# Kernel optimization log

Measured on AMD Instinct MI355X. Metric: run time of the kernel, lower is better.

Reference implementation:

```python
import jax, jax.numpy as jnp
import numpy as np

DIM = 128
HEADS = 4
GN_GROUPS = 4
EPS = 1e-5


def setup_inputs() -> dict:
    key = jax.random.key(0)
    ks = jax.random.split(key, 6)
    B, C, H, W = 4, DIM, 64, 64
    x = jax.random.normal(ks[0], (B, C, H, W), dtype=jnp.float32)
    # 1x1 convs are channel matmuls: store as [out_ch, in_ch]
    w_qkv = jax.random.normal(ks[1], (3 * C, C), dtype=jnp.float32) * (C ** -0.5)
    w_out = jax.random.normal(ks[2], (C, C), dtype=jnp.float32) * (C ** -0.5)
    b_out = jax.random.normal(ks[3], (C,), dtype=jnp.float32) * 0.01
    gn_gamma = jnp.ones((C,), dtype=jnp.float32)
    gn_beta = jnp.zeros((C,), dtype=jnp.float32)
    return {"x": x, "w_qkv": w_qkv, "w_out": w_out, "b_out": b_out,
            "gn_gamma": gn_gamma, "gn_beta": gn_beta}


def _attention_block(x, w_qkv, w_out, b_out, gn_gamma, gn_beta):
    b, c, h, w = x.shape
    d = c // HEADS
    scale = d ** -0.5
    # 1x1 conv == per-pixel matmul over channels
    qkv = jnp.einsum('bchw,oc->bohw', x, w_qkv)  # [b, 3c, h, w]
    q, k, v = jnp.split(qkv, 3, axis=1)
    # 'b (h d) x y -> b h (x y) d'
    def to_heads(t):
        return t.reshape(b, HEADS, d, h * w).transpose(0, 1, 3, 2)  # [b, H, N, d]
    q, k, v = to_heads(q), to_heads(k), to_heads(v)
    dots = jnp.einsum('bhnd,bhmd->bhnm', q, k) * scale  # [b, H, N, N]
    attn = jax.nn.softmax(dots, axis=-1)
    out = jnp.einsum('bhnm,bhmd->bhnd', attn, v)  # [b, H, N, d]
    # 'b h (x y) d -> b (h d) x y'
    out = out.transpose(0, 1, 3, 2).reshape(b, c, h, w)
    # output 1x1 conv + bias
    out = jnp.einsum('bchw,oc->bohw', out, w_out) + b_out[None, :, None, None]
    # GroupNorm(4, c)
    g = out.reshape(b, GN_GROUPS, c // GN_GROUPS, h, w)
    mean = g.mean(axis=(2, 3, 4), keepdims=True)
    var = g.var(axis=(2, 3, 4), keepdims=True)
    g = (g - mean) * jax.lax.rsqrt(var + EPS)
    out = g.reshape(b, c, h, w) * gn_gamma[None, :, None, None] + gn_beta[None, :, None, None]
    return out + x


def reference(x, w_qkv, w_out, b_out, gn_gamma, gn_beta):
    return _attention_block(x, w_qkv, w_out, b_out, gn_gamma, gn_beta)
```

## Files before the change

kernel.cpp:

```cpp
#include <hip/hip_runtime.h>

#define DIM   128
#define NPIX  4096
#define DHEAD 32

using u16 = unsigned short;
typedef __attribute__((ext_vector_type(8))) short   short8;
typedef __attribute__((ext_vector_type(8))) u16     ushort8;
typedef __attribute__((ext_vector_type(4))) float   floatx4;
typedef __attribute__((ext_vector_type(2))) unsigned int uint2v;

#define SCL 0.25513899f

__device__ __forceinline__ float bf2f(u16 u) {
  union { unsigned int i; float f; } v; v.i = ((unsigned int)u) << 16; return v.f;
}
__device__ __forceinline__ u16 f2bf(float f) {
  union { unsigned int i; float f; } v; v.f = f;
  unsigned int i = v.i;
  return (u16)((i + 0x7FFFu + ((i >> 16) & 1u)) >> 16);
}
__device__ __forceinline__ unsigned int pk2bf(float a, float b) {
  union { float f; unsigned int u; } ua, ub; ua.f = a; ub.f = b;
  return __builtin_amdgcn_perm(ub.u, ua.u, 0x07060302u);
}

template<bool F32> __device__ __forceinline__ float ld1(const void* p, size_t i) {
  if constexpr (F32) return ((const float*)p)[i];
  else               return bf2f(((const u16*)p)[i]);
}
template<bool F32> __device__ __forceinline__ float4 ld4(const void* p, size_t i) {
  if constexpr (F32) {
    return *(const float4*)((const float*)p + i);
  } else {
    const ushort4 u = *(const ushort4*)((const u16*)p + i);
    return make_float4(bf2f(u.x), bf2f(u.y), bf2f(u.z), bf2f(u.w));
  }
}
template<bool F32> __device__ __forceinline__ void st4(void* p, size_t i, float4 v) {
  if constexpr (F32) {
    *(float4*)((float*)p + i) = v;
  } else {
    ushort4 u; u.x = f2bf(v.x); u.y = f2bf(v.y); u.z = f2bf(v.z); u.w = f2bf(v.w);
    *(ushort4*)((u16*)p + i) = u;
  }
}

__global__ void k_detect(const u16* __restrict__ x, int* __restrict__ flag,
                         float* __restrict__ S) {
  if (threadIdx.x < 40) S[threadIdx.x] = 0.f;
  if (threadIdx.x == 0 && blockIdx.x == 0) {
    int big = 0;
    for (int i = 0; i < 128; ++i) {
      const float v = bf2f(x[i]);
      if (!(fabsf(v) < 1e4f)) big = 1;
    }
    *flag = big;
  }
}

template<bool F32>
__global__ __launch_bounds__(256) void k_qkv(const void* __restrict__ x,
                                             const void* __restrict__ wqkv,
                                             u16* __restrict__ Q,
                                             u16* __restrict__ K,
                                             u16* __restrict__ V,
                                             const int* __restrict__ flag) {
  if (*flag != (F32 ? 1 : 0)) return;
  const int b = blockIdx.z, y = blockIdx.y, pt = blockIdx.x;
  const int tl = threadIdx.x;
  __shared__ float Ws[32 * 129];
  if (y < 8) {
    const int m = y >> 2, h = y & 3;
    const int ddq = tl & 3, pw = tl >> 2;
    const int rb = m * DIM + h * 32;
    for (int i = tl; i < 32 * DIM; i += 256)
      Ws[(i >> 7) * 129 + (i & 127)] =
          ld1<F32>(wqkv, (size_t)(rb + (i >> 7)) * DIM + (i & 127));
    __syncthreads();
    const int p0 = pt * 256 + pw * 4;
    float acc[8][4];
#pragma unroll
    for (int j = 0; j < 8; ++j) { acc[j][0] = acc[j][1] = acc[j][2] = acc[j][3] = 0.f; }
    const size_t xb = (size_t)b * DIM * NPIX + p0;
    for (int c = 0; c < DIM; ++c) {
      const float4 xv = ld4<F32>(x, xb + (size_t)c * NPIX);
#pragma unroll
      for (int j = 0; j < 8; ++j) {
        const float wv = Ws[(ddq * 8 + j) * 129 + c];
        acc[j][0] += wv * xv.x; acc[j][1] += wv * xv.y;
        acc[j][2] += wv * xv.z; acc[j][3] += wv * xv.w;
      }
    }
    u16* dst = (m == 0) ? Q : K;
    const float scl = (m == 0) ? 1.f : SCL;
    const int bh = b * 4 + h;
#pragma unroll
    for (int t = 0; t < 4; ++t) {
      ushort8 w8;
#pragma unroll
      for (int j = 0; j < 8; ++j) w8[j] = f2bf(acc[j][t] * scl);
      *(ushort8*)(dst + ((size_t)bh * NPIX + p0 + t) * DHEAD + ddq * 8) = w8;
    }
  } else {
    const int og = (y - 8) * 4 + (pt >> 2);
    const int ptv = pt & 3;
    for (int i = tl; i < 8 * DIM; i += 256)
      Ws[(i >> 7) * 129 + (i & 127)] =
          ld1<F32>(wqkv, (size_t)(2 * DIM + og * 8 + (i >> 7)) * DIM + (i & 127));
    __syncthreads();
    const int p0 = ptv * 1024 + tl * 4;
    float acc[8][4];
#pragma unroll
    for (int j = 0; j < 8; ++j) { acc[j][0] = acc[j][1] = acc[j][2] = acc[j][3] = 0.f; }
    const size_t xb = (size_t)b * DIM * NPIX + p0;
    for (int c = 0; c < DIM; ++c) {
      const float4 xv = ld4<F32>(x, xb + (size_t)c * NPIX);
#pragma unroll
      for (int j = 0; j < 8; ++j) {
        const float wv = Ws[j * 129 + c];
        acc[j][0] += wv * xv.x; acc[j][1] += wv * xv.y;
        acc[j][2] += wv * xv.z; acc[j][3] += wv * xv.w;
      }
    }
#pragma unroll
    for (int j = 0; j < 8; ++j) {
      const int c = og * 8 + j;
      ushort4 w4;
      w4.x = f2bf(acc[j][0]); w4.y = f2bf(acc[j][1]);
      w4.z = f2bf(acc[j][2]); w4.w = f2bf(acc[j][3]);
      *(ushort4*)(V + ((size_t)b * DIM + c) * NPIX + p0) = w4;
    }
  }
}

__device__ __forceinline__ short8 xform_p(unsigned c0, unsigned c1,
                                          unsigned c2, unsigned c3) {
  uint2v sw = __builtin_amdgcn_permlane32_swap(c0, c2, false, false);
  uint2v sx = __builtin_amdgcn_permlane16_swap(sw[0], sw[1], false, false);
  uint2v sy = __builtin_amdgcn_permlane32_swap(c1, c3, false, false);
  uint2v sz = __builtin_amdgcn_permlane16_swap(sy[0], sy[1], false, false);
  union { unsigned u[4]; short8 s; } r;
  r.u[0] = sx[0]; r.u[1] = sz[0]; r.u[2] = sx[1]; r.u[3] = sz[1];
  return r.s;
}

__global__ __launch_bounds__(512) void k_attn(const u16* __restrict__ Q,
                                              const u16* __restrict__ K,
                                              const u16* __restrict__ V,
                                              u16* __restrict__ O) {
  const int id = blockIdx.y * 32 + blockIdx.x;
  const int nid = (id & 7) * 64 + (id >> 3);
  const int bh = nid >> 5, qb = nid & 31;
  const int tid = threadIdx.x;
  const int wv = tid >> 6, lane = tid & 63;
  const int quad = lane >> 4, l15 = lane & 15;
  const int b = bh >> 2, h = bh & 3;

  __shared__ __align__(16) u16 Klds[2][128 * 40];
  __shared__ __align__(16) u16 Vlds[2][32 * 136];
  __shared__ __align__(16) u16 Olds[32 * 136];

  const int qtok0 = qb * 128 + wv * 16 + l15;
  const short8 qf = *(const short8*)(Q + ((size_t)bh * NPIX + qtok0) * DHEAD + quad * 8);

  floatx4 o00 = {0.f, 0.f, 0.f, 0.f}, o01 = {0.f, 0.f, 0.f, 0.f};
  floatx4 ol  = {0.f, 0.f, 0.f, 0.f};
  const short8 onesf = {(short)0x3F80, (short)0x3F80, (short)0x3F80, (short)0x3F80,
                        (short)0x3F80, (short)0x3F80, (short)0x3F80, (short)0x3F80};

  const int st = tid & 255;
  const bool isK = tid < 256;
  const int skey = st >> 2, sqt = st & 3;
  const int sdd = st >> 3, soc = st & 7;
  const u16* Gg = isK ? (K + ((size_t)bh * NPIX + skey) * DHEAD + sqt * 8)
                      : (V + ((size_t)(b * DIM + h * DHEAD + sdd)) * NPIX + soc * 8);
  u16* Ld0 = isK ? (Klds[0] + skey * 40 + sqt * 8) : (Vlds[0] + sdd * 136 + soc * 8);
  u16* Ld1 = isK ? (Klds[1] + skey * 40 + sqt * 8) : (Vlds[1] + sdd * 136 + soc * 8);
  const size_t gstep = isK ? (size_t)(128 * DHEAD) : (size_t)128;
  const size_t goff2 = isK ? (size_t)(64 * DHEAD)  : (size_t)64;
  const int    loff2 = isK ? (64 * 40) : 64;

  *(ushort8*)Ld0           = *(const ushort8*)Gg;
  *(ushort8*)(Ld0 + loff2) = *(const ushort8*)(Gg + goff2);

  for (int ch = 0; ch < 32; ++ch) {
    const int cur = ch & 1;
    __syncthreads();
    ushort8 pre0, pre1;
    if (ch + 1 < 32) {
      const u16* gb = Gg + (size_t)(ch + 1) * gstep;
      pre0 = *(const ushort8*)gb;
      pre1 = *(const ushort8*)(gb + goff2);
    }
#pragma unroll
    for (int kc = 0; kc < 4; ++kc) {
      unsigned ca[4];
#pragma unroll
      for (int s = 0; s < 2; ++s) {
        const int sub = kc * 2 + s;
        const short8 af = *(const short8*)(Klds[cur] + (sub * 16 + l15) * 40 + quad * 8);
        const floatx4 s0 = __builtin_amdgcn_mfma_f32_16x16x32_bf16(
            af, qf, (floatx4){0.f, 0.f, 0.f, 0.f}, 0, 0, 0);
        const float a0 = __builtin_amdgcn_exp2f(s0[0]);
        const float a1 = __builtin_amdgcn_exp2f(s0[1]);
        const float a2 = __builtin_amdgcn_exp2f(s0[2]);
        const float a3 = __builtin_amdgcn_exp2f(s0[3]);
        ca[s * 2 + 0] = pk2bf(a0, a1); ca[s * 2 + 1] = pk2bf(a2, a3);
      }
      const short8 pa = xform_p(ca[0], ca[1], ca[2], ca[3]);
      const short8 vb0 = *(const short8*)(Vlds[cur] + l15 * 136 + kc * 32 + quad * 8);
      const short8 vb1 = *(const short8*)(Vlds[cur] + (16 + l15) * 136 + kc * 32 + quad * 8);
      __builtin_amdgcn_s_setprio(1);
      o00 = __builtin_amdgcn_mfma_f32_16x16x32_bf16(pa, vb0, o00, 0, 0, 0);
      o01 = __builtin_amdgcn_mfma_f32_16x16x32_bf16(pa, vb1, o01, 0, 0, 0);
      ol  = __builtin_amdgcn_mfma_f32_16x16x32_bf16(pa, onesf, ol, 0, 0, 0);
      __builtin_amdgcn_s_setprio(0);
    }
    if (ch + 1 < 32) {
      u16* dst = cur ? Ld0 : Ld1;
      *(ushort8*)dst           = pre0;
      *(ushort8*)(dst + loff2) = pre1;
    }
  }
  float li[4];
#pragma unroll
  for (int r = 0; r < 4; ++r) li[r] = 1.f / ol[r];
  uint2v w00, w01;
  w00[0] = (unsigned)f2bf(o00[0] * li[0]) | ((unsigned)f2bf(o00[1] * li[1]) << 16);
  w00[1] = (unsigned)f2bf(o00[2] * li[2]) | ((unsigned)f2bf(o00[3] * li[3]) << 16);
  w01[0] = (unsigned)f2bf(o01[0] * li[0]) | ((unsigned)f2bf(o01[1] * li[1]) << 16);
  w01[1] = (unsigned)f2bf(o01[2] * li[2]) | ((unsigned)f2bf(o01[3] * li[3]) << 16);
  __syncthreads();
  *(uint2v*)(Olds + l15 * 136 + wv * 16 + quad * 4) = w00;
  *(uint2v*)(Olds + (16 + l15) * 136 + wv * 16 + quad * 4) = w01;
  __syncthreads();
  const int d = tid >> 4, oc = tid & 15;
  u16* og = O + ((size_t)(b * DIM + h * DHEAD + d)) * NPIX + qb * 128;
  *(ushort8*)(og + oc * 8) = *(const ushort8*)(Olds + d * 136 + oc * 8);
}

template<bool F32>
__global__ __launch_bounds__(256) void k_proj(const u16* __restrict__ O,
                                              const void* __restrict__ wout,
                                              const void* __restrict__ bout,
                                              float* __restrict__ Y,
                                              float* __restrict__ Sred,
                                              const int* __restrict__ flag) {
  if (*flag != (F32 ? 1 : 0)) return;
  const int b = blockIdx.z, og = blockIdx.y, pt = blockIdx.x;
  const int tl = threadIdx.x;
  __shared__ float Ws[8][DIM];
  for (int i = tl; i < 8 * DIM; i += 256)
    Ws[i >> 7][i & 127] = ld1<F32>(wout, (size_t)(og * 8 + (i >> 7)) * DIM + (i & 127));
  __syncthreads();
  const int p0 = pt * 512 + tl * 2;
  float acc[8][2];
#pragma unroll
  for (int j = 0; j < 8; ++j) { acc[j][0] = acc[j][1] = 0.f; }
  const u16* Ob = O + (size_t)b * DIM * NPIX + p0;
  for (int c = 0; c < DIM; ++c) {
    const ushort2 xv2 = *(const ushort2*)(Ob + (size_t)c * NPIX);
    const float x0 = bf2f(xv2.x), x1 = bf2f(xv2.y);
#pragma unroll
    for (int j = 0; j < 8; ++j) {
      const float wv = Ws[j][c];
      acc[j][0] += wv * x0; acc[j][1] += wv * x1;
    }
  }
  float s1 = 0.f, s2 = 0.f;
#pragma unroll
  for (int j = 0; j < 8; ++j) {
    const int o = og * 8 + j;
    const float bo = ld1<F32>(bout, o);
    float2 y2;
    y2.x = acc[j][0] + bo; y2.y = acc[j][1] + bo;
    *(float2*)(Y + ((size_t)b * DIM + o) * NPIX + p0) = y2;
    s1 += y2.x + y2.y;
    s2 += y2.x * y2.x + y2.y * y2.y;
  }
  __shared__ float red[2][256];
  red[0][tl] = s1; red[1][tl] = s2;
  __syncthreads();
  for (int off = 128; off >= 1; off >>= 1) {
    if (tl < off) { red[0][tl] += red[0][tl + off]; red[1][tl] += red[1][tl + off]; }
    __syncthreads();
  }
  if (tl == 0) {
    const int g = og >> 2;
    atomicAdd(&Sred[(b * 4 + g) * 2 + 0], red[0][0]);
    atomicAdd(&Sred[(b * 4 + g) * 2 + 1], red[1][0]);
  }
}

template<bool F32>
__global__ __launch_bounds__(256) void k_gn(const float* __restrict__ Y,
                                            const float* __restrict__ Sred,
                                            const void* __restrict__ x,
                                            const void* __restrict__ gamma,
                                            const void* __restrict__ beta,
                                            void* __restrict__ out,
                                            const int* __restrict__ flag) {
  if (*flag != (F32 ? 1 : 0)) return;
  const int idx = (blockIdx.x * 256 + threadIdx.x) * 4;
  const int b = idx >> 19;
  const int c = (idx >> 12) & 127;
  const int g = c >> 5;
  const float inv_n = 1.f / (32.f * 4096.f);
  const float s1 = Sred[(b * 4 + g) * 2 + 0];
  const float s2 = Sred[(b * 4 + g) * 2 + 1];
  const float mean = s1 * inv_n;
  const float var = s2 * inv_n - mean * mean;
  const float rs = rsqrtf(var + 1e-5f);
  const float ga = ld1<F32>(gamma, c) * rs;
  const float be = ld1<F32>(beta, c) - mean * ga;
  const float4 y4 = *(const float4*)(Y + idx);
  const float4 xv = ld4<F32>(x, idx);
  float4 r;
  r.x = y4.x * ga + be + xv.x;
  r.y = y4.y * ga + be + xv.y;
  r.z = y4.z * ga + be + xv.z;
  r.w = y4.w * ga + be + xv.w;
  st4<F32>(out, idx, r);
}

extern "C" void kernel_launch(void* const* d_in, const int* in_sizes, int n_in,
                              void* d_out, int out_size, void* d_ws, size_t ws_size,
                              hipStream_t stream) {
  const void* x     = d_in[0];
  const void* wqkv  = d_in[1];
  const void* wout  = d_in[2];
  const void* bout  = d_in[3];
  const void* gamma = d_in[4];
  const void* beta  = d_in[5];
  char* ws = (char*)d_ws;
  u16*   Q = (u16*)(ws + ((size_t)0  << 20));
  u16*   K = (u16*)(ws + ((size_t)8  << 20));
  u16*   V = (u16*)(ws + ((size_t)16 << 20));
  u16*   O = (u16*)(ws + ((size_t)24 << 20));
  float* Y = (float*)(ws + ((size_t)32 << 20));
  float* S = (float*)(ws + ((size_t)40 << 20));
  int*   F = (int*)(ws + ((size_t)40 << 20) + 128);

  k_detect<<<1, 64, 0, stream>>>((const u16*)x, F, S);

  k_qkv<false><<<dim3(16, 12, 4), 256, 0, stream>>>(x, wqkv, Q, K, V, F);
  k_qkv<true> <<<dim3(16, 12, 4), 256, 0, stream>>>(x, wqkv, Q, K, V, F);
  k_attn<<<dim3(32, 16), 512, 0, stream>>>(Q, K, V, O);
  k_proj<false><<<dim3(8, 16, 4), 256, 0, stream>>>(O, wout, bout, Y, S, F);
  k_proj<true> <<<dim3(8, 16, 4), 256, 0, stream>>>(O, wout, bout, Y, S, F);
  k_gn<false><<<2048, 256, 0, stream>>>(Y, S, x, gamma, beta, d_out, F);
  k_gn<true> <<<2048, 256, 0, stream>>>(Y, S, x, gamma, beta, d_out, F);
}
```

Measured before the change: 180.4 us.

## Fuse GroupNorm and residual into projection kernel with grid-wide atomic barrier

Drops the separate GroupNorm kernel and the fp32 intermediate Y buffer. The projection kernel keeps its outputs in registers and publishes group sums by atomics. Each block then spins on a global counter until all 512 blocks have contributed, and applies normalization, gamma/beta and the residual before writing the output directly. This removes a full round trip of the projection output through global memory plus one launch. In exchange it relies on all 512 blocks being co-resident to avoid deadlock, and adds spin-wait latency.

Result: slower. 210.7 us (+16.8%).

```diff
diff --git a/kernel.cpp b/kernel.cpp
--- a/kernel.cpp
+++ b/kernel.cpp
@@ -37,12 +37,20 @@
     return make_float4(bf2f(u.x), bf2f(u.y), bf2f(u.z), bf2f(u.w));
   }
 }
-template<bool F32> __device__ __forceinline__ void st4(void* p, size_t i, float4 v) {
+template<bool F32> __device__ __forceinline__ float2 ld2(const void* p, size_t i) {
   if constexpr (F32) {
-    *(float4*)((float*)p + i) = v;
+    return *(const float2*)((const float*)p + i);
   } else {
-    ushort4 u; u.x = f2bf(v.x); u.y = f2bf(v.y); u.z = f2bf(v.z); u.w = f2bf(v.w);
-    *(ushort4*)((u16*)p + i) = u;
+    const ushort2 u = *(const ushort2*)((const u16*)p + i);
+    return make_float2(bf2f(u.x), bf2f(u.y));
+  }
+}
+template<bool F32> __device__ __forceinline__ void st2(void* p, size_t i, float2 v) {
+  if constexpr (F32) {
+    *(float2*)((float*)p + i) = v;
+  } else {
+    ushort2 u; u.x = f2bf(v.x); u.y = f2bf(v.y);
+    *(ushort2*)((u16*)p + i) = u;
   }
 }
 
@@ -244,8 +252,12 @@
 __global__ __launch_bounds__(256) void k_proj(const u16* __restrict__ O,
                                               const void* __restrict__ wout,
                                               const void* __restrict__ bout,
-                                              float* __restrict__ Y,
+                                              const void* __restrict__ x,
+                                              const void* __restrict__ gamma,
+                                              const void* __restrict__ beta,
+                                              void* __restrict__ out,
                                               float* __restrict__ Sred,
+                                              int* __restrict__ Ctr,
                                               const int* __restrict__ flag) {
   if (*flag != (F32 ? 1 : 0)) return;
   const int b = blockIdx.z, og = blockIdx.y, pt = blockIdx.x;
@@ -271,13 +283,10 @@
   float s1 = 0.f, s2 = 0.f;
 #pragma unroll
   for (int j = 0; j < 8; ++j) {
-    const int o = og * 8 + j;
-    const float bo = ld1<F32>(bout, o);
-    float2 y2;
-    y2.x = acc[j][0] + bo; y2.y = acc[j][1] + bo;
-    *(float2*)(Y + ((size_t)b * DIM + o) * NPIX + p0) = y2;
-    s1 += y2.x + y2.y;
-    s2 += y2.x * y2.x + y2.y * y2.y;
+    const float bo = ld1<F32>(bout, og * 8 + j);
+    acc[j][0] += bo; acc[j][1] += bo;
+    s1 += acc[j][0] + acc[j][1];
+    s2 += acc[j][0] * acc[j][0] + acc[j][1] * acc[j][1];
   }
   __shared__ float red[2][256];
   red[0][tl] = s1; red[1][tl] = s2;
@@ -286,42 +295,35 @@
     if (tl < off) { red[0][tl] += red[0][tl + off]; red[1][tl] += red[1][tl + off]; }
     __syncthreads();
   }
+  const int g = og >> 2;
   if (tl == 0) {
-    const int g = og >> 2;
     atomicAdd(&Sred[(b * 4 + g) * 2 + 0], red[0][0]);
     atomicAdd(&Sred[(b * 4 + g) * 2 + 1], red[1][0]);
-  }
-}
-
-template<bool F32>
-__global__ __launch_bounds__(256) void k_gn(const float* __restrict__ Y,
-                                            const float* __restrict__ Sred,
-                                            const void* __restrict__ x,
-                                            const void* __restrict__ gamma,
-                                            const void* __restrict__ beta,
-                                            void* __restrict__ out,
-                                            const int* __restrict__ flag) {
-  if (*flag != (F32 ? 1 : 0)) return;
-  const int idx = (blockIdx.x * 256 + threadIdx.x) * 4;
-  const int b = idx >> 19;
-  const int c = (idx >> 12) & 127;
-  const int g = c >> 5;
+    __threadfence();
+    atomicAdd(Ctr, 1);
+    while (__hip_atomic_load(Ctr, __ATOMIC_ACQUIRE, __HIP_MEMORY_SCOPE_AGENT) < 512) {}
+    red[0][0] = __hip_atomic_load(&Sred[(b * 4 + g) * 2 + 0],
+                                  __ATOMIC_RELAXED, __HIP_MEMORY_SCOPE_AGENT);
+    red[1][0] = __hip_atomic_load(&Sred[(b * 4 + g) * 2 + 1],
+                                  __ATOMIC_RELAXED, __HIP_MEMORY_SCOPE_AGENT);
+  }
+  __syncthreads();
   const float inv_n = 1.f / (32.f * 4096.f);
-  const float s1 = Sred[(b * 4 + g) * 2 + 0];
-  const float s2 = Sred[(b * 4 + g) * 2 + 1];
-  const float mean = s1 * inv_n;
-  const float var = s2 * inv_n - mean * mean;
+  const float mean = red[0][0] * inv_n;
+  const float var  = red[1][0] * inv_n - mean * mean;
   const float rs = rsqrtf(var + 1e-5f);
-  const float ga = ld1<F32>(gamma, c) * rs;
-  const float be = ld1<F32>(beta, c) - mean * ga;
-  const float4 y4 = *(const float4*)(Y + idx);
-  const float4 xv = ld4<F32>(x, idx);
-  float4 r;
-  r.x = y4.x * ga + be + xv.x;
-  r.y = y4.y * ga + be + xv.y;
-  r.z = y4.z * ga + be + xv.z;
-  r.w = y4.w * ga + be + xv.w;
-  st4<F32>(out, idx, r);
+#pragma unroll
+  for (int j = 0; j < 8; ++j) {
+    const int c = og * 8 + j;
+    const float ga = ld1<F32>(gamma, c) * rs;
+    const float be = ld1<F32>(beta, c) - mean * ga;
+    const size_t xi = ((size_t)b * DIM + c) * NPIX + p0;
+    const float2 xv = ld2<F32>(x, xi);
+    float2 r;
+    r.x = acc[j][0] * ga + be + xv.x;
+    r.y = acc[j][1] * ga + be + xv.y;
+    st2<F32>(out, xi, r);
+  }
 }
 
 extern "C" void kernel_launch(void* const* d_in, const int* in_sizes, int n_in,
@@ -338,17 +340,17 @@
   u16*   K = (u16*)(ws + ((size_t)8  << 20));
   u16*   V = (u16*)(ws + ((size_t)16 << 20));
   u16*   O = (u16*)(ws + ((size_t)24 << 20));
-  float* Y = (float*)(ws + ((size_t)32 << 20));
   float* S = (float*)(ws + ((size_t)40 << 20));
   int*   F = (int*)(ws + ((size_t)40 << 20) + 128);
+  int*   C = (int*)(ws + ((size_t)40 << 20) + 132);
 
   k_detect<<<1, 64, 0, stream>>>((const u16*)x, F, S);
 
   k_qkv<false><<<dim3(16, 12, 4), 256, 0, stream>>>(x, wqkv, Q, K, V, F);
   k_qkv<true> <<<dim3(16, 12, 4), 256, 0, stream>>>(x, wqkv, Q, K, V, F);
   k_attn<<<dim3(32, 16), 512, 0, stream>>>(Q, K, V, O);
-  k_proj<false><<<dim3(8, 16, 4), 256, 0, stream>>>(O, wout, bout, Y, S, F);
-  k_proj<true> <<<dim3(8, 16, 4), 256, 0, stream>>>(O, wout, bout, Y, S, F);
-  k_gn<false><<<2048, 256, 0, stream>>>(Y, S, x, gamma, beta, d_out, F);
-  k_gn<true> <<<2048, 256, 0, stream>>>(Y, S, x, gamma, beta, d_out, F);
-}
+  k_proj<false><<<dim3(8, 16, 4), 256, 0, stream>>>(O, wout, bout, x, gamma, beta,
+                                                    d_out, S, C, F);
+  k_proj<true> <<<dim3(8, 16, 4), 256, 0, stream>>>(O, wout, bout, x, gamma, beta,
+                                                    d_out, S, C, F);
+}
```
